# Kernel tuning notes

Measured on AMD Instinct MI355X. Metric: run time of the kernel, lower is better.

Reference implementation:

```python
import jax, jax.numpy as jnp
import numpy as np

N = 100000   # nodes
E = 3200000  # edges (avg degree 32)
G = 64       # graphs in batch
H = 64       # hidden channels
EPS = 1e-5   # BatchNorm eps


def setup_inputs() -> dict:
    key = jax.random.key(0)
    ks = jax.random.split(key, 32)
    rn = lambda k, s: jax.random.normal(k, s, jnp.float32) * 0.1
    inp = {
        "x": jax.random.normal(ks[0], (N, 3), jnp.float32),
        "edge_index": jax.random.randint(ks[1], (2, E), 0, N),
        "batch": jnp.sort(jax.random.randint(ks[2], (N,), 0, G)),
    }
    dims = [(3, H), (H, H), (H, H)]
    for i, (di, do) in enumerate(dims):
        inp[f"W{i}"] = rn(ks[3 + i], (di, do))
        inp[f"b{i}"] = jnp.zeros((do,), jnp.float32)
        inp[f"g{i}"] = jnp.ones((do,), jnp.float32)
        inp[f"beta{i}"] = jnp.zeros((do,), jnp.float32)
    for j, p in enumerate(["p", "a", "t"]):
        out = 2 if p == "t" else 1
        inp[p + "W1"] = rn(ks[8 + 2 * j], (H, H // 2))
        inp[p + "b1"] = jnp.zeros((H // 2,), jnp.float32)
        inp[p + "W2"] = rn(ks[9 + 2 * j], (H // 2, out))
        inp[p + "b2"] = jnp.zeros((out,), jnp.float32)
    return inp


def _forward(x, edge_index, batch, params):
    (W0, b0, g0, beta0, W1, b1, g1, beta1, W2, b2, g2, beta2,
     pW1, pb1, pW2, pb2, aW1, ab1, aW2, ab2, tW1, tb1, tW2, tb2) = params
    src, dst = edge_index[0], edge_index[1]
    # GCN normalization with self-loops: deg = in-degree + 1
    deg = jax.ops.segment_sum(jnp.ones((E,), x.dtype), dst, num_segments=N) + 1.0
    dis = jax.lax.rsqrt(deg)  # deg^{-1/2}

    def gcn(h_in, W, b):
        h = h_in @ W  # [N, H]
        msg = h[src] * (dis[src] * dis[dst])[:, None]  # [E, H] gather
        out = jax.ops.segment_sum(msg, dst, num_segments=N)  # scatter-add
        out = out + h * (dis * dis)[:, None]  # self-loop term
        return out + b

    def bn_relu(h, g, be):
        m = jnp.mean(h, axis=0)
        v = jnp.var(h, axis=0)  # biased, as torch BN training mode
        return jax.nn.relu(g * (h - m) * jax.lax.rsqrt(v + EPS) + be)

    for W, b, g, be in [(W0, b0, g0, beta0), (W1, b1, g1, beta1), (W2, b2, g2, beta2)]:
        x = bn_relu(gcn(x, W, b), g, be)

    # global_mean_pool over graphs
    counts = jax.ops.segment_sum(jnp.ones((N,), x.dtype), batch, num_segments=G)
    pooled = jax.ops.segment_sum(x, batch, num_segments=G) / jnp.maximum(counts, 1.0)[:, None]

    def head(Wa, ba, Wb, bb):
        return jax.nn.relu(pooled @ Wa + ba) @ Wb + bb

    power = head(pW1, pb1, pW2, pb2)   # [G, 1]
    area = head(aW1, ab1, aW2, ab2)    # [G, 1]
    timing = head(tW1, tb1, tW2, tb2)  # [G, 2] = (tns, wns)
    return jnp.concatenate([power, area, timing], axis=1)  # [G, 4]


def reference(x, edge_index, batch, W0, b0, g0, beta0, W1, b1, g1, beta1,
              W2, b2, g2, beta2, pW1, pb1, pW2, pb2, aW1, ab1, aW2, ab2,
              tW1, tb1, tW2, tb2):
    params = (W0, b0, g0, beta0, W1, b1, g1, beta1, W2, b2, g2, beta2,
              pW1, pb1, pW2, pb2, aW1, ab1, aW2, ab2, tW1, tb1, tW2, tb2)
    return _forward(x, edge_index, batch, params)
```

## Files before the change

### kernel.cpp

```cpp
#include <hip/hip_runtime.h>
#include <hip/hip_fp16.h>

#define EPSBN 1e-5f
#define SH 7
#define CHUNK 16384
#define SCANB 256

__launch_bounds__(1024)
__global__ void k_hist(const int* __restrict__ dst, int* __restrict__ hist,
                       int E, int C, int NB) {
    __shared__ int h[1024];
    const int tid = threadIdx.x, c = blockIdx.x;
    for (int i = tid; i < NB; i += 1024) h[i] = 0;
    __syncthreads();
    const int e0 = c * CHUNK, e1 = min(e0 + CHUNK, E);
    for (int e = e0 + tid; e < e1; e += 1024) atomicAdd(&h[dst[e] >> SH], 1);
    __syncthreads();
    for (int b = tid; b < NB; b += 1024) hist[b * C + c] = h[b];
}

__launch_bounds__(256)
__global__ void k_scanA(const int* __restrict__ hist, int* __restrict__ bsum, int M) {
    __shared__ int part[256];
    const int b = blockIdx.x, t = threadIdx.x;
    const int seg = (M + SCANB - 1) / SCANB;
    const int lo = b * seg, hi = min(lo + seg, M);
    int s = 0;
    for (int i = lo + t; i < hi; i += 256) s += hist[i];
    part[t] = s;
    __syncthreads();
    for (int d = 128; d > 0; d >>= 1) {
        if (t < d) part[t] += part[t + d];
        __syncthreads();
    }
    if (t == 0) bsum[b] = part[0];
}

__launch_bounds__(256)
__global__ void k_scanB(int* __restrict__ bsum, float* __restrict__ st,
                        float* __restrict__ poolsum, float* __restrict__ counts, int G) {
    __shared__ int sh[256];
    const int t = threadIdx.x;
    sh[t] = bsum[t];
    __syncthreads();
    for (int d = 1; d < 256; d <<= 1) {
        int v = (t >= d) ? sh[t - d] : 0;
        __syncthreads();
        sh[t] += v;
        __syncthreads();
    }
    bsum[t] = (t == 0) ? 0 : sh[t - 1];
    for (int i = t; i < 3 * 128; i += 256) st[i] = 0.f;
    for (int i = t; i < G * 64; i += 256) poolsum[i] = 0.f;
    for (int i = t; i < G; i += 256) counts[i] = 0.f;
}

__launch_bounds__(256)
__global__ void k_scanC(int* __restrict__ hist, const int* __restrict__ bsum,
                        int* __restrict__ off, int M, int E, int N) {
    __shared__ int part[256];
    const int b = blockIdx.x, t = threadIdx.x;
    const int seg = (M + SCANB - 1) / SCANB;
    const int lo = b * seg, hi = min(lo + seg, M);
    const int per = (seg + 255) >> 8;
    const int tl = lo + t * per, th = min(tl + per, hi);
    int s = 0;
    for (int i = tl; i < th; ++i) s += hist[i];
    part[t] = s;
    __syncthreads();
    for (int d = 1; d < 256; d <<= 1) {
        int v = (t >= d) ? part[t - d] : 0;
        __syncthreads();
        part[t] += v;
        __syncthreads();
    }
    int run = bsum[b] + ((t == 0) ? 0 : part[t - 1]);
    for (int i = tl; i < th; ++i) {
        int v = hist[i];
        hist[i] = run;
        run += v;
    }
    if (b == 0 && t == 0) off[N] = E;
}

__launch_bounds__(1024)
__global__ void k_sort(const int* __restrict__ src, const int* __restrict__ dst,
                       const int* __restrict__ hist, int* __restrict__ spk,
                       int E, int C, int NB) {
    __shared__ int cur[1024];
    const int tid = threadIdx.x, c = blockIdx.x;
    for (int b = tid; b < NB; b += 1024) cur[b] = hist[b * C + c];
    __syncthreads();
    const int e0 = c * CHUNK, e1 = min(e0 + CHUNK, E);
    for (int e = e0 + tid; e < e1; e += 1024) {
        const int d = dst[e];
        const int pos = atomicAdd(&cur[d >> SH], 1);
        spk[pos] = ((d & 127) << 18) | src[e];
    }
}

__launch_bounds__(256)
__global__ void k_csr(const int* __restrict__ spk, const int* __restrict__ hist,
                      const float* __restrict__ x0, int* __restrict__ off,
                      float* __restrict__ dis, float4* __restrict__ x0s4,
                      int* __restrict__ eda, int E, int C, int NB, int N) {
    __shared__ int cnt_l[128], scn[128];
    const int tid = threadIdx.x, b = blockIdx.x;
    const int node0 = b << SH;
    const int nloc = min(128, N - node0);
    const int ebeg = hist[b * C];
    const int eend = (b + 1 < NB) ? hist[(b + 1) * C] : E;
    if (tid < 128) cnt_l[tid] = 0;
    __syncthreads();
    for (int e = ebeg + tid; e < eend; e += 256) {
        atomicAdd(&cnt_l[spk[e] >> 18], 1);
    }
    __syncthreads();
    if (tid < 128) scn[tid] = cnt_l[tid];
    __syncthreads();
    for (int d = 1; d < 128; d <<= 1) {
        int v = 0;
        if (tid < 128 && tid >= d) v = scn[tid - d];
        __syncthreads();
        if (tid < 128) scn[tid] += v;
        __syncthreads();
    }
    if (tid < nloc) {
        const int excl = scn[tid] - cnt_l[tid];
        const int i = node0 + tid;
        const float d = rsqrtf((float)cnt_l[tid] + 1.0f);
        off[i] = ebeg + excl;
        dis[i] = d;
        x0s4[i] = make_float4(d * x0[3 * i], d * x0[3 * i + 1], d * x0[3 * i + 2], 0.f);
    }
    __syncthreads();
    if (tid < 128) cnt_l[tid] = scn[tid] - cnt_l[tid];
    __syncthreads();
    for (int e = ebeg + tid; e < eend; e += 256) {
        const int p = spk[e];
        const int r = atomicAdd(&cnt_l[p >> 18], 1);
        eda[ebeg + r] = p & 0x3FFFF;
    }
}

__launch_bounds__(256)
__global__ void k_gl0(const int* __restrict__ off, const int* __restrict__ eda,
                      const float* __restrict__ dis, const float4* __restrict__ x0s4,
                      const float* __restrict__ W0, __half* __restrict__ bufh,
                      float* __restrict__ st, int N) {
    __shared__ float Ws[192];
    __shared__ float ls[256], lq[256];
    const int tid = threadIdx.x;
    const int lane = tid & 63, wv = tid >> 6;
    for (int i = tid; i < 192; i += 256) Ws[i] = W0[i];
    __syncthreads();
    const int nw = gridDim.x * 4;
    float s = 0.f, q = 0.f;
    for (int w = blockIdx.x * 4 + wv; w < N; w += nw) {
        const int e0 = off[w], e1 = off[w + 1];
        float a0 = 0.f, a1 = 0.f, a2 = 0.f;
        for (int e = e0 + lane; e < e1; e += 64) {
            float4 v = x0s4[eda[e]];
            a0 += v.x;
            a1 += v.y;
            a2 += v.z;
        }
#pragma unroll
        for (int d = 32; d; d >>= 1) {
            a0 += __shfl_xor(a0, d);
            a1 += __shfl_xor(a1, d);
            a2 += __shfl_xor(a2, d);
        }
        const float4 sv = x0s4[w];
        const float dw = dis[w];
        const float z0 = dw * (a0 + sv.x), z1 = dw * (a1 + sv.y), z2 = dw * (a2 + sv.z);
        const float val = z0 * Ws[lane] + z1 * Ws[64 + lane] + z2 * Ws[128 + lane];
        bufh[((long)w << 6) + lane] = __float2half(val);
        s += val;
        q = fmaf(val, val, q);
    }
    ls[tid] = s;
    lq[tid] = q;
    __syncthreads();
    if (tid < 64) {
        s = ls[lane] + ls[lane + 64] + ls[lane + 128] + ls[lane + 192];
        q = lq[lane] + lq[lane + 64] + lq[lane + 128] + lq[lane + 192];
        unsafeAtomicAdd(&st[lane], s);
        unsafeAtomicAdd(&st[64 + lane], q);
    }
}

__launch_bounds__(256)
__global__ void k_linear(const __half* __restrict__ X, const float* __restrict__ W,
                         const float* __restrict__ st, const float* __restrict__ g,
                         const float* __restrict__ be, const float* __restrict__ dis,
                         __half* __restrict__ hp, int N) {
    __shared__ float Ws[64 * 64];
    __shared__ float Xs[32 * 64];
    __shared__ float scs[64], shs[64];
    const int tid = threadIdx.x;
    if (tid < 64) {
        const float inv = 1.0f / (float)N;
        const float m = st[tid] * inv;
        const float v = st[64 + tid] * inv - m * m;
        const float sc = g[tid] * rsqrtf(v + EPSBN);
        scs[tid] = sc;
        shs[tid] = fmaf(-m, sc, be[tid]);
    }
    for (int i = tid; i < 64 * 64; i += 256) Ws[i] = W[i];
    __syncthreads();
    const int c = tid & 63, wv = tid >> 6;
    for (int r0 = blockIdx.x * 32; r0 < N; r0 += gridDim.x * 32) {
        for (int i = tid; i < 32 * 32; i += 256) {
            const int r = i >> 5, c2 = i & 31;
            const int row = r0 + r;
            float2 f = {0.f, 0.f};
            if (row < N) {
                const __half2 hv = ((const __half2*)X)[((long)row << 5) + c2];
                f = __half22float2(hv);
            }
            const int ch = c2 * 2;
            Xs[r * 64 + ch] = fmaxf(fmaf(f.x, scs[ch], shs[ch]), 0.f);
            Xs[r * 64 + ch + 1] = fmaxf(fmaf(f.y, scs[ch + 1], shs[ch + 1]), 0.f);
        }
        __syncthreads();
        for (int rr = 0; rr < 8; ++rr) {
            const int r = wv * 8 + rr;
            const int row = r0 + r;
            if (row < N) {
                float acc = 0.f;
#pragma unroll
                for (int k = 0; k < 64; ++k) acc = fmaf(Xs[r * 64 + k], Ws[k * 64 + c], acc);
                hp[(long)row * 64 + c] = __float2half(acc * dis[row]);
            }
        }
        __syncthreads();
    }
}

__launch_bounds__(256)
__global__ void k_gather(const int* __restrict__ off, const int* __restrict__ eda,
                         const float* __restrict__ dis, const __half* __restrict__ hp,
                         __half* __restrict__ aggh, float* __restrict__ st, int N) {
    __shared__ int els[4][2][64];
    __shared__ float ls[256], ls2[256];
    const int lane = threadIdx.x & 63;
    const int wv = threadIdx.x >> 6;
    const int nwaves = gridDim.x * 4;
    const int P = (N + 1) >> 1;
    float s = 0.f, s2 = 0.f;
    for (int p = blockIdx.x * 4 + wv; p < P; p += nwaves) {
        const int wA = p, wB = p + P;
        const bool hasB = (wB < N);
        const int a0o = off[wA];
        const int nA = off[wA + 1] - a0o;
        const int b0o = hasB ? off[wB] : 0;
        const int nB = hasB ? off[wB + 1] - b0o : 0;
        float accA0 = __half2float(hp[(long)wA * 64 + lane]);
        float accA1 = 0.f, accA2 = 0.f, accA3 = 0.f;
        float accB0 = hasB ? __half2float(hp[(long)wB * 64 + lane]) : 0.f;
        float accB1 = 0.f, accB2 = 0.f, accB3 = 0.f;
        int rA = (lane < nA) ? eda[a0o + lane] : 0;
        int rB = (lane < nB) ? eda[b0o + lane] : 0;
        const int nmax = nA > nB ? nA : nB;
        for (int base = 0; base < nmax; base += 64) {
            els[wv][0][lane] = rA;
            els[wv][1][lane] = rB;
            const int nxt = base + 64;
            if (nxt + lane < nA) rA = eda[a0o + nxt + lane];
            if (nxt + lane < nB) rB = eda[b0o + nxt + lane];
            int mA = nA - base;
            mA = mA < 0 ? 0 : (mA > 64 ? 64 : mA);
            int mB = nB - base;
            mB = mB < 0 ? 0 : (mB > 64 ? 64 : mB);
            const int mc = mA < mB ? mA : mB;
            int j = 0;
            for (; j + 4 <= mc; j += 4) {
                const int sa0 = els[wv][0][j + 0], sa1 = els[wv][0][j + 1];
                const int sa2 = els[wv][0][j + 2], sa3 = els[wv][0][j + 3];
                const int sb0 = els[wv][1][j + 0], sb1 = els[wv][1][j + 1];
                const int sb2 = els[wv][1][j + 2], sb3 = els[wv][1][j + 3];
                const float va0 = __half2float(hp[(long)sa0 * 64 + lane]);
                const float va1 = __half2float(hp[(long)sa1 * 64 + lane]);
                const float va2 = __half2float(hp[(long)sa2 * 64 + lane]);
                const float va3 = __half2float(hp[(long)sa3 * 64 + lane]);
                const float vb0 = __half2float(hp[(long)sb0 * 64 + lane]);
                const float vb1 = __half2float(hp[(long)sb1 * 64 + lane]);
                const float vb2 = __half2float(hp[(long)sb2 * 64 + lane]);
                const float vb3 = __half2float(hp[(long)sb3 * 64 + lane]);
                accA0 += va0;
                accA1 += va1;
                accA2 += va2;
                accA3 += va3;
                accB0 += vb0;
                accB1 += vb1;
                accB2 += vb2;
                accB3 += vb3;
            }
            int jA = j, jB = j;
            for (; jA + 4 <= mA; jA += 4) {
                const int sa0 = els[wv][0][jA + 0], sa1 = els[wv][0][jA + 1];
                const int sa2 = els[wv][0][jA + 2], sa3 = els[wv][0][jA + 3];
                const float va0 = __half2float(hp[(long)sa0 * 64 + lane]);
                const float va1 = __half2float(hp[(long)sa1 * 64 + lane]);
                const float va2 = __half2float(hp[(long)sa2 * 64 + lane]);
                const float va3 = __half2float(hp[(long)sa3 * 64 + lane]);
                accA0 += va0;
                accA1 += va1;
                accA2 += va2;
                accA3 += va3;
            }
            for (; jA < mA; ++jA) accA0 += __half2float(hp[(long)els[wv][0][jA] * 64 + lane]);
            for (; jB + 4 <= mB; jB += 4) {
                const int sb0 = els[wv][1][jB + 0], sb1 = els[wv][1][jB + 1];
                const int sb2 = els[wv][1][jB + 2], sb3 = els[wv][1][jB + 3];
                const float vb0 = __half2float(hp[(long)sb0 * 64 + lane]);
                const float vb1 = __half2float(hp[(long)sb1 * 64 + lane]);
                const float vb2 = __half2float(hp[(long)sb2 * 64 + lane]);
                const float vb3 = __half2float(hp[(long)sb3 * 64 + lane]);
                accB0 += vb0;
                accB1 += vb1;
                accB2 += vb2;
                accB3 += vb3;
            }
            for (; jB < mB; ++jB) accB0 += __half2float(hp[(long)els[wv][1][jB] * 64 + lane]);
        }
        const float outA = dis[wA] * ((accA0 + accA1) + (accA2 + accA3));
        aggh[((long)wA << 6) + lane] = __float2half(outA);
        s += outA;
        s2 = fmaf(outA, outA, s2);
        if (hasB) {
            const float outB = dis[wB] * ((accB0 + accB1) + (accB2 + accB3));
            aggh[((long)wB << 6) + lane] = __float2half(outB);
            s += outB;
            s2 = fmaf(outB, outB, s2);
        }
    }
    ls[threadIdx.x] = s;
    ls2[threadIdx.x] = s2;
    __syncthreads();
    if (threadIdx.x < 64) {
        s = ls[lane] + ls[lane + 64] + ls[lane + 128] + ls[lane + 192];
        s2 = ls2[lane] + ls2[lane + 64] + ls2[lane + 128] + ls2[lane + 192];
        unsafeAtomicAdd(&st[lane], s);
        unsafeAtomicAdd(&st[64 + lane], s2);
    }
}

__launch_bounds__(256)
__global__ void k_pool(const __half* __restrict__ x, const int* __restrict__ batch,
                       const float* __restrict__ st, const float* __restrict__ g,
                       const float* __restrict__ be, float* __restrict__ poolsum,
                       float* __restrict__ counts, int N, int npw) {
    const int wid = (blockIdx.x * blockDim.x + threadIdx.x) >> 6;
    const int lane = threadIdx.x & 63;
    const int n0 = wid * npw;
    if (n0 >= N) return;
    const float inv = 1.0f / (float)N;
    const float m = st[lane] * inv;
    const float v = st[64 + lane] * inv - m * m;
    const float sc = g[lane] * rsqrtf(v + EPSBN);
    const float sh = fmaf(-m, sc, be[lane]);
    const int n1 = min(n0 + npw, N);
    float acc = 0.f, cnt = 0.f;
    int gr = batch[n0];
    for (int n = n0; n < n1; ++n) {
        int gn = batch[n];
        if (gn != gr) {
            unsafeAtomicAdd(&poolsum[(long)gr * 64 + lane], acc);
            if (lane == 0) unsafeAtomicAdd(&counts[gr], cnt);
            acc = 0.f;
            cnt = 0.f;
            gr = gn;
        }
        const float val = __half2float(x[((long)n << 6) + lane]);
        acc += fmaxf(fmaf(val, sc, sh), 0.f);
        cnt += 1.f;
    }
    unsafeAtomicAdd(&poolsum[(long)gr * 64 + lane], acc);
    if (lane == 0) unsafeAtomicAdd(&counts[gr], cnt);
}

__launch_bounds__(256)
__global__ void k_heads(const float* __restrict__ poolsum, const float* __restrict__ counts,
                        const float* pW1, const float* pb1, const float* pW2, const float* pb2,
                        const float* aW1, const float* ab1, const float* aW2, const float* ab2,
                        const float* tW1, const float* tb1, const float* tW2, const float* tb2,
                        float* __restrict__ out, int G) {
    __shared__ float P[64 * 64];
    __shared__ float Hd[64 * 32];
    const int tid = threadIdx.x;
    for (int i = tid; i < G * 64; i += 256) {
        int g = i >> 6;
        P[i] = poolsum[i] / fmaxf(counts[g], 1.f);
    }
    __syncthreads();
    for (int j = 0; j < 3; ++j) {
        const float* W1 = (j == 0) ? pW1 : (j == 1) ? aW1 : tW1;
        const float* b1 = (j == 0) ? pb1 : (j == 1) ? ab1 : tb1;
        const float* W2 = (j == 0) ? pW2 : (j == 1) ? aW2 : tW2;
        const float* b2 = (j == 0) ? pb2 : (j == 1) ? ab2 : tb2;
        for (int i = tid; i < G * 32; i += 256) {
            int g = i >> 5, k = i & 31;
            float a = b1[k];
#pragma unroll
            for (int c = 0; c < 64; ++c) a = fmaf(P[g * 64 + c], W1[c * 32 + k], a);
            Hd[i] = fmaxf(a, 0.f);
        }
        __syncthreads();
        const int ow = (j == 2) ? 2 : 1;
        const int off = (j == 2) ? 2 : j;
        for (int i = tid; i < G * ow; i += 256) {
            int g = i / ow, o = i - g * ow;
            float a = b2[o];
#pragma unroll
            for (int k = 0; k < 32; ++k) a = fmaf(Hd[g * 32 + k], W2[k * ow + o], a);
            out[g * 4 + off + o] = a;
        }
        __syncthreads();
    }
}

extern "C" void kernel_launch(void* const* d_in, const int* in_sizes, int n_in,
                              void* d_out, int out_size, void* d_ws, size_t ws_size,
                              hipStream_t stream) {
    const int N = in_sizes[2];
    const int E = in_sizes[1] / 2;
    const int G = out_size / 4;

    const float* x0 = (const float*)d_in[0];
    const int* ei = (const int*)d_in[1];
    const int* src = ei;
    const int* dst = ei + E;
    const int* batch = (const int*)d_in[2];

    const float* W[3] = {(const float*)d_in[3], (const float*)d_in[7], (const float*)d_in[11]};
    const float* gam[3] = {(const float*)d_in[5], (const float*)d_in[9], (const float*)d_in[13]};
    const float* bet[3] = {(const float*)d_in[6], (const float*)d_in[10], (const float*)d_in[14]};

    const float* pW1 = (const float*)d_in[15];
    const float* pb1 = (const float*)d_in[16];
    const float* pW2 = (const float*)d_in[17];
    const float* pb2 = (const float*)d_in[18];
    const float* aW1 = (const float*)d_in[19];
    const float* ab1 = (const float*)d_in[20];
    const float* aW2 = (const float*)d_in[21];
    const float* ab2 = (const float*)d_in[22];
    const float* tW1 = (const float*)d_in[23];
    const float* tb1 = (const float*)d_in[24];
    const float* tW2 = (const float*)d_in[25];
    const float* tb2 = (const float*)d_in[26];

    const int C = (E + CHUNK - 1) / CHUNK;
    const int NB = (N + 127) >> SH;
    const int M = NB * C;

    auto align = [](size_t x) { return (x + 255) & ~(size_t)255; };
    char* w = (char*)d_ws;
    float* dis = (float*)w;      w += align((size_t)N * 4);
    __half* bufh = (__half*)w;   w += align((size_t)N * 64 * 2);
    __half* hp = (__half*)w;     w += align((size_t)N * 64 * 2);
    float* st = (float*)w;       w += align(3 * 128 * 4);
    float* poolsum = (float*)w;  w += align((size_t)G * 64 * 4);
    float* counts = (float*)w;   w += align((size_t)G * 4);
    int* off = (int*)w;          w += align((size_t)(N + 1) * 4);
    int* hist = (int*)w;         w += align((size_t)M * 4);
    int* bsum = (int*)w;         w += align((size_t)SCANB * 4);
    int* spk = (int*)w;          w += align((size_t)E * 4);
    int* eda = (int*)w;          w += align((size_t)E * 4);
    float4* x0s4 = (float4*)w;   w += align((size_t)N * 16);
    (void)ws_size;

    const int nb_ga = 2048;

    k_hist<<<C, 1024, 0, stream>>>(dst, hist, E, C, NB);
    k_scanA<<<SCANB, 256, 0, stream>>>(hist, bsum, M);
    k_scanB<<<1, 256, 0, stream>>>(bsum, st, poolsum, counts, G);
    k_scanC<<<SCANB, 256, 0, stream>>>(hist, bsum, off, M, E, N);
    k_sort<<<C, 1024, 0, stream>>>(src, dst, hist, spk, E, C, NB);
    k_csr<<<NB, 256, 0, stream>>>(spk, hist, x0, off, dis, x0s4, eda, E, C, NB, N);

    k_gl0<<<2048, 256, 0, stream>>>(off, eda, dis, x0s4, W[0], bufh, st, N);

    for (int l = 1; l < 3; ++l) {
        k_linear<<<1024, 256, 0, stream>>>(bufh, W[l], st + (l - 1) * 128,
                                           gam[l - 1], bet[l - 1], dis, hp, N);
        k_gather<<<nb_ga, 256, 0, stream>>>(off, eda, dis, hp, bufh, st + l * 128, N);
    }

    const int npw = 32;
    const int nwaves = (N + npw - 1) / npw;
    const int nb_pool = (nwaves * 64 + 255) / 256;
    k_pool<<<nb_pool, 256, 0, stream>>>(bufh, batch, st + 256, gam[2], bet[2],
                                        poolsum, counts, N, npw);

    k_heads<<<1, 256, 0, stream>>>(poolsum, counts, pW1, pb1, pW2, pb2,
                                   aW1, ab1, aW2, ab2, tW1, tb1, tW2, tb2,
                                   (float*)d_out, G);
}
```

Measured before the change: 473.1 us.

## Split neighbor gather into source-index bands for cache locality

```diff
diff --git a/kernel.cpp b/kernel.cpp
--- a/kernel.cpp
+++ b/kernel.cpp
@@ -102,21 +102,31 @@
 __launch_bounds__(256)
 __global__ void k_csr(const int* __restrict__ spk, const int* __restrict__ hist,
                       const float* __restrict__ x0, int* __restrict__ off,
-                      float* __restrict__ dis, float4* __restrict__ x0s4,
-                      int* __restrict__ eda, int E, int C, int NB, int N) {
+                      int* __restrict__ bnd, float* __restrict__ dis,
+                      float4* __restrict__ x0s4, int* __restrict__ eda,
+                      int E, int C, int NB, int N, float invw) {
+    __shared__ int cnt4[512];
     __shared__ int cnt_l[128], scn[128];
     const int tid = threadIdx.x, b = blockIdx.x;
     const int node0 = b << SH;
     const int nloc = min(128, N - node0);
     const int ebeg = hist[b * C];
     const int eend = (b + 1 < NB) ? hist[(b + 1) * C] : E;
-    if (tid < 128) cnt_l[tid] = 0;
+    for (int i = tid; i < 512; i += 256) cnt4[i] = 0;
     __syncthreads();
     for (int e = ebeg + tid; e < eend; e += 256) {
-        atomicAdd(&cnt_l[spk[e] >> 18], 1);
-    }
-    __syncthreads();
-    if (tid < 128) scn[tid] = cnt_l[tid];
+        const int p = spk[e];
+        const int loc = p >> 18;
+        const int s = p & 0x3FFFF;
+        const int band = min(3, (int)((float)s * invw));
+        atomicAdd(&cnt4[(loc << 2) | band], 1);
+    }
+    __syncthreads();
+    if (tid < 128) {
+        cnt_l[tid] = cnt4[tid << 2] + cnt4[(tid << 2) | 1] + cnt4[(tid << 2) | 2] +
+                     cnt4[(tid << 2) | 3];
+        scn[tid] = cnt_l[tid];
+    }
     __syncthreads();
     for (int d = 1; d < 128; d <<= 1) {
         int v = 0;
@@ -126,20 +136,29 @@
         __syncthreads();
     }
     if (tid < nloc) {
-        const int excl = scn[tid] - cnt_l[tid];
+        const int start = scn[tid] - cnt_l[tid];
         const int i = node0 + tid;
         const float d = rsqrtf((float)cnt_l[tid] + 1.0f);
-        off[i] = ebeg + excl;
+        off[i] = ebeg + start;
         dis[i] = d;
         x0s4[i] = make_float4(d * x0[3 * i], d * x0[3 * i + 1], d * x0[3 * i + 2], 0.f);
-    }
-    __syncthreads();
-    if (tid < 128) cnt_l[tid] = scn[tid] - cnt_l[tid];
+        int run = start;
+#pragma unroll
+        for (int bb = 0; bb < 4; ++bb) {
+            const int cc = cnt4[(tid << 2) | bb];
+            bnd[((long)i << 2) | bb] = ebeg + run;
+            cnt4[(tid << 2) | bb] = run;
+            run += cc;
+        }
+    }
     __syncthreads();
     for (int e = ebeg + tid; e < eend; e += 256) {
         const int p = spk[e];
-        const int r = atomicAdd(&cnt_l[p >> 18], 1);
-        eda[ebeg + r] = p & 0x3FFFF;
+        const int loc = p >> 18;
+        const int s = p & 0x3FFFF;
+        const int band = min(3, (int)((float)s * invw));
+        const int r = atomicAdd(&cnt4[(loc << 2) | band], 1);
+        eda[ebeg + r] = s;
     }
 }
 
@@ -239,26 +258,30 @@
 }
 
 __launch_bounds__(256)
-__global__ void k_gather(const int* __restrict__ off, const int* __restrict__ eda,
-                         const float* __restrict__ dis, const __half* __restrict__ hp,
-                         __half* __restrict__ aggh, float* __restrict__ st, int N) {
+__global__ void k_gb(const int* __restrict__ off, const int* __restrict__ bnd,
+                     const int* __restrict__ eda, const float* __restrict__ dis,
+                     const __half* __restrict__ hp, float* __restrict__ accf,
+                     __half* __restrict__ bufh, float* __restrict__ st,
+                     int N, int band, int lastband) {
     __shared__ int els[4][2][64];
     __shared__ float ls[256], ls2[256];
     const int lane = threadIdx.x & 63;
     const int wv = threadIdx.x >> 6;
     const int nwaves = gridDim.x * 4;
     const int P = (N + 1) >> 1;
+    const bool first = (band == 0);
+    const bool last = (band == lastband);
     float s = 0.f, s2 = 0.f;
     for (int p = blockIdx.x * 4 + wv; p < P; p += nwaves) {
         const int wA = p, wB = p + P;
         const bool hasB = (wB < N);
-        const int a0o = off[wA];
-        const int nA = off[wA + 1] - a0o;
-        const int b0o = hasB ? off[wB] : 0;
-        const int nB = hasB ? off[wB + 1] - b0o : 0;
-        float accA0 = __half2float(hp[(long)wA * 64 + lane]);
+        const int a0o = bnd[((long)wA << 2) | band];
+        const int nA = (last ? off[wA + 1] : bnd[((long)wA << 2) | (band + 1)]) - a0o;
+        const int b0o = hasB ? bnd[((long)wB << 2) | band] : 0;
+        const int nB = hasB ? (last ? off[wB + 1] : bnd[((long)wB << 2) | (band + 1)]) - b0o : 0;
+        float accA0 = first ? __half2float(hp[(long)wA * 64 + lane]) : 0.f;
         float accA1 = 0.f, accA2 = 0.f, accA3 = 0.f;
-        float accB0 = hasB ? __half2float(hp[(long)wB * 64 + lane]) : 0.f;
+        float accB0 = (first && hasB) ? __half2float(hp[(long)wB * 64 + lane]) : 0.f;
         float accB1 = 0.f, accB2 = 0.f, accB3 = 0.f;
         int rA = (lane < nA) ? eda[a0o + lane] : 0;
         int rB = (lane < nB) ? eda[b0o + lane] : 0;
@@ -325,25 +348,43 @@
             }
             for (; jB < mB; ++jB) accB0 += __half2float(hp[(long)els[wv][1][jB] * 64 + lane]);
         }
-        const float outA = dis[wA] * ((accA0 + accA1) + (accA2 + accA3));
-        aggh[((long)wA << 6) + lane] = __float2half(outA);
-        s += outA;
-        s2 = fmaf(outA, outA, s2);
-        if (hasB) {
-            const float outB = dis[wB] * ((accB0 + accB1) + (accB2 + accB3));
-            aggh[((long)wB << 6) + lane] = __float2half(outB);
-            s += outB;
-            s2 = fmaf(outB, outB, s2);
-        }
-    }
-    ls[threadIdx.x] = s;
-    ls2[threadIdx.x] = s2;
-    __syncthreads();
-    if (threadIdx.x < 64) {
-        s = ls[lane] + ls[lane + 64] + ls[lane + 128] + ls[lane + 192];
-        s2 = ls2[lane] + ls2[lane + 64] + ls2[lane + 128] + ls2[lane + 192];
-        unsafeAtomicAdd(&st[lane], s);
-        unsafeAtomicAdd(&st[64 + lane], s2);
+        const float pA = (accA0 + accA1) + (accA2 + accA3);
+        const float pB = (accB0 + accB1) + (accB2 + accB3);
+        const long iA = ((long)wA << 6) + lane;
+        const long iB = ((long)wB << 6) + lane;
+        if (!last) {
+            if (first) {
+                accf[iA] = pA;
+                if (hasB) accf[iB] = pB;
+            } else {
+                accf[iA] += pA;
+                if (hasB) accf[iB] += pB;
+            }
+        } else {
+            const float tA = (first ? 0.f : accf[iA]) + pA;
+            const float outA = dis[wA] * tA;
+            bufh[iA] = __float2half(outA);
+            s += outA;
+            s2 = fmaf(outA, outA, s2);
+            if (hasB) {
+                const float tB = (first ? 0.f : accf[iB]) + pB;
+                const float outB = dis[wB] * tB;
+                bufh[iB] = __float2half(outB);
+                s += outB;
+                s2 = fmaf(outB, outB, s2);
+            }
+        }
+    }
+    if (last) {
+        ls[threadIdx.x] = s;
+        ls2[threadIdx.x] = s2;
+        __syncthreads();
+        if (threadIdx.x < 64) {
+            s = ls[lane] + ls[lane + 64] + ls[lane + 128] + ls[lane + 192];
+            s2 = ls2[lane] + ls2[lane + 64] + ls2[lane + 128] + ls2[lane + 192];
+            unsafeAtomicAdd(&st[lane], s);
+            unsafeAtomicAdd(&st[64 + lane], s2);
+        }
     }
 }
 
@@ -454,16 +495,21 @@
     const int C = (E + CHUNK - 1) / CHUNK;
     const int NB = (N + 127) >> SH;
     const int M = NB * C;
+    const int wid = (N + 3) >> 2;
+    const float invw = 1.0f / (float)wid;
+    const int nbands = 4;
 
     auto align = [](size_t x) { return (x + 255) & ~(size_t)255; };
     char* w = (char*)d_ws;
     float* dis = (float*)w;      w += align((size_t)N * 4);
     __half* bufh = (__half*)w;   w += align((size_t)N * 64 * 2);
     __half* hp = (__half*)w;     w += align((size_t)N * 64 * 2);
+    float* accf = (float*)w;     w += align((size_t)N * 64 * 4);
     float* st = (float*)w;       w += align(3 * 128 * 4);
     float* poolsum = (float*)w;  w += align((size_t)G * 64 * 4);
     float* counts = (float*)w;   w += align((size_t)G * 4);
     int* off = (int*)w;          w += align((size_t)(N + 1) * 4);
+    int* bnd = (int*)w;          w += align((size_t)N * 4 * 4);
     int* hist = (int*)w;         w += align((size_t)M * 4);
     int* bsum = (int*)w;         w += align((size_t)SCANB * 4);
     int* spk = (int*)w;          w += align((size_t)E * 4);
@@ -471,21 +517,21 @@
     float4* x0s4 = (float4*)w;   w += align((size_t)N * 16);
     (void)ws_size;
 
-    const int nb_ga = 2048;
-
     k_hist<<<C, 1024, 0, stream>>>(dst, hist, E, C, NB);
     k_scanA<<<SCANB, 256, 0, stream>>>(hist, bsum, M);
     k_scanB<<<1, 256, 0, stream>>>(bsum, st, poolsum, counts, G);
     k_scanC<<<SCANB, 256, 0, stream>>>(hist, bsum, off, M, E, N);
     k_sort<<<C, 1024, 0, stream>>>(src, dst, hist, spk, E, C, NB);
-    k_csr<<<NB, 256, 0, stream>>>(spk, hist, x0, off, dis, x0s4, eda, E, C, NB, N);
+    k_csr<<<NB, 256, 0, stream>>>(spk, hist, x0, off, bnd, dis, x0s4, eda, E, C, NB, N, invw);
 
     k_gl0<<<2048, 256, 0, stream>>>(off, eda, dis, x0s4, W[0], bufh, st, N);
 
     for (int l = 1; l < 3; ++l) {
         k_linear<<<1024, 256, 0, stream>>>(bufh, W[l], st + (l - 1) * 128,
                                            gam[l - 1], bet[l - 1], dis, hp, N);
-        k_gather<<<nb_ga, 256, 0, stream>>>(off, eda, dis, hp, bufh, st + l * 128, N);
+        for (int bb = 0; bb < nbands; ++bb)
+            k_gb<<<2048, 256, 0, stream>>>(off, bnd, eda, dis, hp, accf, bufh,
+                                           st + l * 128, N, bb, nbands - 1);
     }
 
     const int npw = 32;
```

Measured after the change: 597.1 us. +26.2%, slower.
